# Optimization experiments

Hardware: AMD Instinct MI355X
Metric: run time of the kernel (lower is better)

## Reference

```python
import jax, jax.numpy as jnp
import numpy as np

# geomloss SamplesLoss('sinkhorn', p=2, blur=0.05, scaling=0.5, debias=True) math
P = 2
BLUR = 0.05
SCALING = 0.5
DIAMETER = 64.0  # static conservative bound on point-cloud diameter for randn D=64 data


def _eps_schedule():
    eps_list = []
    e = DIAMETER ** P
    target = BLUR ** P
    while e > target:
        eps_list.append(e)
        e *= SCALING ** P
    eps_list.append(target)
    return np.array(eps_list, dtype=np.float32)


def _cost(x, y):
    # C_ij = ||x_i - y_j||^2 / 2   (p=2 cost of geomloss)
    sq = (jnp.sum(x * x, -1)[:, :, None] * 0.5
          + jnp.sum(y * y, -1)[:, None, :] * 0.5
          - jnp.einsum('bnd,bmd->bnm', x, y))
    return jnp.maximum(sq, 0.0)


def _softmin(eps, C, h):
    # f_i = -eps * log sum_j exp(h_j - C_ij / eps);  C: (B,N,M), h: (B,M)
    return -eps * jax.nn.logsumexp(h[:, None, :] - C / eps, axis=-1)


def setup_inputs() -> dict:
    key = jax.random.key(0)
    k1, k2, k3, k4 = jax.random.split(key, 4)
    B, N, M, D = 8, 2048, 2048, 64
    x = jax.random.normal(k1, (B, N, D), dtype=jnp.float32)
    y = jax.random.normal(k2, (B, M, D), dtype=jnp.float32)
    w1 = jax.random.uniform(k3, (B, N), dtype=jnp.float32) + 0.01
    w2 = jax.random.uniform(k4, (B, M), dtype=jnp.float32) + 0.01
    w1 = w1 / jnp.sum(w1, axis=-1, keepdims=True)
    w2 = w2 / jnp.sum(w2, axis=-1, keepdims=True)
    return {'x': x, 'y': y, 'w1': w1, 'w2': w2}


def _sinkhorn_divergence(x, y, w1, w2):
    a_log = jnp.log(w1)
    b_log = jnp.log(w2)
    eps_list = jnp.asarray(_eps_schedule())

    # --- Sinkhorn loop on detached quantities (geomloss detaches the loop) ---
    xd = jax.lax.stop_gradient(x)
    yd = jax.lax.stop_gradient(y)
    ald = jax.lax.stop_gradient(a_log)
    bld = jax.lax.stop_gradient(b_log)
    C_xy_d = _cost(xd, yd)
    C_yx_d = jnp.swapaxes(C_xy_d, 1, 2)
    C_xx_d = _cost(xd, xd)
    C_yy_d = _cost(yd, yd)

    eps0 = eps_list[0]
    f_ab = _softmin(eps0, C_xy_d, bld)
    g_ba = _softmin(eps0, C_yx_d, ald)
    f_aa = _softmin(eps0, C_xx_d, ald)
    g_bb = _softmin(eps0, C_yy_d, bld)

    def step(carry, eps):
        f_ab, g_ba, f_aa, g_bb = carry
        ft = _softmin(eps, C_xy_d, bld + g_ba / eps)
        gt = _softmin(eps, C_yx_d, ald + f_ab / eps)
        f_aa_t = _softmin(eps, C_xx_d, ald + f_aa / eps)
        g_bb_t = _softmin(eps, C_yy_d, bld + g_bb / eps)
        return (0.5 * (f_ab + ft), 0.5 * (g_ba + gt),
                0.5 * (f_aa + f_aa_t), 0.5 * (g_bb + g_bb_t)), None

    (f_ab, g_ba, f_aa, g_bb), _ = jax.lax.scan(step, (f_ab, g_ba, f_aa, g_bb), eps_list)

    # --- last extrapolation at eps = blur^p, differentiable ---
    eps = eps_list[-1]
    C_xy = _cost(x, y)
    C_yx = jnp.swapaxes(C_xy, 1, 2)
    C_xx = _cost(x, x)
    C_yy = _cost(y, y)
    f_ab_f = _softmin(eps, C_xy, b_log + g_ba / eps)
    g_ba_f = _softmin(eps, C_yx, a_log + f_ab / eps)
    f_aa_f = _softmin(eps, C_xx, a_log + f_aa / eps)
    g_bb_f = _softmin(eps, C_yy, b_log + g_bb / eps)

    # debiased sinkhorn cost per batch element
    loss = (jnp.sum(w1 * (f_ab_f - f_aa_f), axis=-1)
            + jnp.sum(w2 * (g_ba_f - g_bb_f), axis=-1))
    return loss


def reference(x, y, w1, w2):
    loss = _sinkhorn_divergence(x, y, w1, w2)
    return jnp.mean(loss)  # reduction='mean'
```

## Files before the change

### kernel.cpp

```cpp
#include <hip/hip_runtime.h>

#define NB 8
#define NN 2048
#define MM 2048
#define DD 64
#define NCHK 16
#define TS 128
#define L2E 1.4426950408889634f
#define LN2 0.6931471805599453f

typedef _Float16 half_t;
typedef __attribute__((ext_vector_type(8))) _Float16 f16x8;
typedef __attribute__((ext_vector_type(4))) float f32x4;
typedef __attribute__((ext_vector_type(2))) float f32x2;

__device__ inline f32x2 lo2(f32x4 v) { return __builtin_shufflevector(v, v, 0, 1); }
__device__ inline f32x2 hi2(f32x4 v) { return __builtin_shufflevector(v, v, 2, 3); }

__device__ half_t g_xh[NB * NN * DD];
__device__ half_t g_yh[NB * MM * DD];
__device__ float g_fab[3][NB * NN], g_gba[3][NB * NN];
__device__ float g_faa[3][NB * NN], g_gbb[3][NB * NN];
__device__ float g_alog[NB * NN], g_blog[NB * NN];
__device__ float g_xn[NB * NN], g_yn[NB * NN];
__device__ float g_h0[NB * MM], g_h1[NB * NN], g_h2[NB * NN], g_h3[NB * MM];
__device__ float2 g_pfab[NB * NCHK * NN];
__device__ float2 g_pgba[NB * NCHK * NN];
__device__ float2 g_pfaa[NB * NCHK * NN];
__device__ float2 g_pgbb[NB * NCHK * NN];

__global__ __launch_bounds__(256) void prep_kernel(
    const float* __restrict__ x, const float* __restrict__ y,
    const float* __restrict__ w1, const float* __restrict__ w2)
{
  int gid = blockIdx.x * 256 + threadIdx.x;
  if (gid < NB * NN) {
    g_alog[gid] = log2f(w1[gid]);
    g_blog[gid] = log2f(w2[gid]);
  }
  int lane = threadIdx.x & 63;
  int row = blockIdx.x * 4 + (threadIdx.x >> 6);
  float xv = x[(size_t)row * DD + lane];
  float yv = y[(size_t)row * DD + lane];
  g_xh[(size_t)row * DD + lane] = (half_t)xv;
  g_yh[(size_t)row * DD + lane] = (half_t)yv;
  float sx = xv * xv;
  float sy = yv * yv;
#pragma unroll
  for (int off = 32; off > 0; off >>= 1) {
    sx += __shfl_down(sx, off);
    sy += __shfl_down(sy, off);
  }
  if (lane == 0) {
    g_xn[row] = 0.5f * sx;
    g_yn[row] = 0.5f * sy;
  }
}

__global__ __launch_bounds__(256) void hprep_kernel(
    const float* __restrict__ fab_in, const float* __restrict__ gba_in,
    const float* __restrict__ faa_in, const float* __restrict__ gbb_in,
    float gs2)
{
  int i = blockIdx.x * 256 + threadIdx.x;
  g_h0[i] = fmaf(gs2, gba_in[i], g_blog[i]);
  g_h1[i] = fmaf(gs2, fab_in[i], g_alog[i]);
  g_h2[i] = fmaf(gs2, faa_in[i], g_alog[i]);
  g_h3[i] = fmaf(gs2, gbb_in[i], g_blog[i]);
}

struct FusedArgs {
  const half_t* Af;
  const half_t* Bf;
  const float* nrow;
  const float* ncol;
  const float* hrow;
  const float* hcol;
  float2* prow;
  float2* pcol;
  int sym;
};

__global__ __launch_bounds__(512) void tile_fused(
    FusedArgs T0, FusedArgs T1, FusedArgs T2, float keps)
{
  int u = blockIdx.x;
  int slab, b, I, J;
  if (u < 2048) {
    slab = 0; b = u >> 8;
    int tt = u & 255; I = tt >> 4; J = tt & 15;
  } else {
    int v = u - 2048;
    slab = 1 + v / 1088;
    int w2 = v % 1088;
    b = w2 / 136;
    int rem = w2 % 136, ii = 0;
    while (rem >= NCHK - ii) { rem -= NCHK - ii; ++ii; }
    I = ii; J = ii + rem;
  }
  FusedArgs A = (slab == 0) ? T0 : (slab == 1) ? T1 : T2;

  const int t = threadIdx.x;
  const int w = t >> 6, lane = t & 63;
  const int m = lane & 15, quad = lane >> 4;
  const int i0 = I * TS, j0 = J * TS;

  __shared__ __align__(16) char sh[33792];
  float* redR = (float*)sh;
  float* redC = (float*)(sh + 8704);
  float* rowM = (float*)(sh + 25600);
  float* colM = (float*)(sh + 26112);
  float* ynkL = (float*)(sh + 32768);
  float* hrL  = (float*)(sh + 33280);

  {
    const char* gA = (const char*)(A.Af + ((size_t)b * NN + i0) * DD);
    const char* gB = (const char*)(A.Bf + ((size_t)b * MM + j0) * DD);
#pragma unroll
    for (int k = 0; k < 4; ++k) {
      int seg = w * 4 + k;
      int p = (seg * 1024 + lane * 16) & 16383;
      int row = p >> 7, colb = p & 127;
      int colx = colb ^ ((row & 7) << 4);
      const char* src = (seg < 16 ? gA : gB) + (size_t)row * 128 + colx;
      __builtin_amdgcn_global_load_lds(
          (const __attribute__((address_space(1))) unsigned int*)src,
          (__attribute__((address_space(3))) unsigned int*)(sh + seg * 1024),
          16, 0, 0);
    }
  }

  if (t < 128) {
    ynkL[t] = -A.ncol[(size_t)b * MM + j0 + t] * keps;
  } else if (t < 256) {
    hrL[t - 128] = A.hrow[(size_t)b * MM + j0 + (t - 128)];
  }
  size_t ro = (size_t)b * NN + i0 + 16 * w + 4 * quad;
  float4 xr = *(const float4*)(A.nrow + ro);
  float4 hq = *(const float4*)(A.hcol + ro);
  f32x2 xnkp0 = {-xr.x * keps, -xr.y * keps};
  f32x2 xnkp1 = {-xr.z * keps, -xr.w * keps};
  f32x2 hcp0 = {hq.x, hq.y}, hcp1 = {hq.z, hq.w};

  __syncthreads();

  const int qb0 = quad * 16, qb1 = qb0 + 64;
  const int ra = 16 * w + m, sa = (ra & 7) << 4;
  f16x8 a0 = *(const f16x8*)(sh + ra * 128 + (qb0 ^ sa));
  f16x8 a1 = *(const f16x8*)(sh + ra * 128 + (qb1 ^ sa));

  const int sb = (m & 7) << 4;
  const char* bb = sh + 16384 + m * 128;
  f32x4 acc[8];
#pragma unroll
  for (int c = 0; c < 8; ++c) {
    f16x8 b0 = *(const f16x8*)(bb + c * 2048 + (qb0 ^ sb));
    f16x8 b1 = *(const f16x8*)(bb + c * 2048 + (qb1 ^ sb));
    f32x4 a = {0.f, 0.f, 0.f, 0.f};
    a = __builtin_amdgcn_mfma_f32_16x16x32_f16(a0, b0, a, 0, 0, 0);
    a = __builtin_amdgcn_mfma_f32_16x16x32_f16(a1, b1, a, 0, 0, 0);
    acc[c] = a;
  }

  __syncthreads();

  const f32x2 kv = {keps, keps};
  const f32x2 zz = {0.f, 0.f};
  f32x2 rmp0 = {-3.0e38f, -3.0e38f}, rmp1 = {-3.0e38f, -3.0e38f};
#pragma unroll
  for (int c = 0; c < 8; ++c) {
    float ynk_c = ynkL[16 * c + m];
    float hr_c = hrL[16 * c + m];
    f32x2 ay0 = xnkp0 + ynk_c;
    f32x2 ay1 = xnkp1 + ynk_c;
    f32x2 q0 = __builtin_elementwise_fma(lo2(acc[c]), kv, ay0);
    f32x2 q1 = __builtin_elementwise_fma(hi2(acc[c]), kv, ay1);
    f32x2 b0 = __builtin_elementwise_min(q0, zz);
    f32x2 b1 = __builtin_elementwise_min(q1, zz);
    acc[c] = __builtin_shufflevector(b0, b1, 0, 1, 2, 3);
    f32x2 rv0 = b0 + hr_c;
    f32x2 rv1 = b1 + hr_c;
    rmp0 = __builtin_elementwise_max(rmp0, rv0);
    rmp1 = __builtin_elementwise_max(rmp1, rv1);
    f32x2 cv0 = b0 + hcp0;
    f32x2 cv1 = b1 + hcp1;
    float cm_c = fmaxf(fmaxf(cv0.x, cv0.y), fmaxf(cv1.x, cv1.y));
    redC[(16 * c + m) * 33 + 4 * w + quad] = cm_c;
  }
  {
    int rbase = (16 * w + 4 * quad) * 17 + m;
    redR[rbase] = rmp0.x; redR[rbase + 17] = rmp0.y;
    redR[rbase + 34] = rmp1.x; redR[rbase + 51] = rmp1.y;
  }
  __syncthreads();

  if (t < 128) {
    float mx = redR[t * 17];
#pragma unroll
    for (int k = 1; k < 16; ++k) mx = fmaxf(mx, redR[t * 17 + k]);
    rowM[t] = mx;
  } else if (t < 256) {
    int cc = t - 128;
    float mx = redC[cc * 33];
#pragma unroll
    for (int k = 1; k < 32; ++k) mx = fmaxf(mx, redC[cc * 33 + k]);
    colM[cc] = mx;
  }
  __syncthreads();

  float4 rq = *(const float4*)(rowM + 16 * w + 4 * quad);
  f32x2 rmv0 = {rq.x, rq.y}, rmv1 = {rq.z, rq.w};
  f32x2 rsp0 = {0.f, 0.f}, rsp1 = {0.f, 0.f};
#pragma unroll
  for (int c = 0; c < 8; ++c) {
    float hr_c = hrL[16 * c + m];
    float cmv_c = colM[16 * c + m];
    f32x2 hrm0 = hr_c - rmv0;
    f32x2 hrm1 = hr_c - rmv1;
    f32x2 chm0 = hcp0 - cmv_c;
    f32x2 chm1 = hcp1 - cmv_c;
    f32x2 b0 = lo2(acc[c]), b1 = hi2(acc[c]);
    f32x2 t0 = b0 + hrm0, t1 = b1 + hrm1;
    float e0 = __builtin_amdgcn_exp2f(t0.x), e1 = __builtin_amdgcn_exp2f(t0.y);
    float e2 = __builtin_amdgcn_exp2f(t1.x), e3 = __builtin_amdgcn_exp2f(t1.y);
    f32x2 ep0 = {e0, e1}, ep1 = {e2, e3};
    rsp0 += ep0; rsp1 += ep1;
    f32x2 u0 = b0 + chm0, u1 = b1 + chm1;
    float f0 = __builtin_amdgcn_exp2f(u0.x), f1 = __builtin_amdgcn_exp2f(u0.y);
    float f2 = __builtin_amdgcn_exp2f(u1.x), f3 = __builtin_amdgcn_exp2f(u1.y);
    redC[(16 * c + m) * 33 + 4 * w + quad] = (f0 + f1) + (f2 + f3);
  }
  {
    int rbase = (16 * w + 4 * quad) * 17 + m;
    redR[rbase] = rsp0.x; redR[rbase + 17] = rsp0.y;
    redR[rbase + 34] = rsp1.x; redR[rbase + 51] = rsp1.y;
  }
  __syncthreads();

  if (t < 128) {
    float s = 0.f;
#pragma unroll
    for (int k = 0; k < 16; ++k) s += redR[t * 17 + k];
    A.prow[((size_t)b * NCHK + J) * NN + i0 + t] = make_float2(rowM[t], s);
  } else if (t < 256) {
    if (!(A.sym && I == J)) {
      int cc = t - 128;
      float s = 0.f;
#pragma unroll
      for (int k = 0; k < 32; ++k) s += redC[cc * 33 + k];
      A.pcol[((size_t)b * NCHK + I) * NN + j0 + cc] = make_float2(colM[cc], s);
    }
  }
}

struct MergeArgs {
  const float2* part;
  const float* fold;
  float* fout;
  const float* hbase;
  float* hout;
};

__global__ __launch_bounds__(256) void merge4(
    MergeArgs M0, MergeArgs M1, MergeArgs M2, MergeArgs M3,
    float eps, float alpha, float beta, float nextgs)
{
  MergeArgs A = (blockIdx.z == 0) ? M0 : (blockIdx.z == 1) ? M1
              : (blockIdx.z == 2) ? M2 : M3;
  const int b = blockIdx.y;
  const int i = blockIdx.x * 256 + threadIdx.x;
  float2 p[NCHK];
#pragma unroll
  for (int k = 0; k < NCHK; ++k)
    p[k] = A.part[((size_t)b * NCHK + k) * NN + i];
  float M = p[0].x;
#pragma unroll
  for (int k = 1; k < NCHK; ++k) M = fmaxf(M, p[k].x);
  float S = 0.f;
#pragma unroll
  for (int k = 0; k < NCHK; ++k) S += p[k].y * __builtin_amdgcn_exp2f(p[k].x - M);
  float ft = (-LN2 * eps) * (M + __log2f(S));
  int idx = b * NN + i;
  float fnew = alpha * A.fold[idx] + beta * ft;
  A.fout[idx] = fnew;
  A.hout[idx] = fmaf(nextgs * L2E, fnew, A.hbase[idx]);
}

__global__ __launch_bounds__(256) void loss_kernel(
    const float* __restrict__ w1, const float* __restrict__ w2,
    float* __restrict__ out)
{
  __shared__ float red[256];
  float acc = 0.f;
  for (int idx = threadIdx.x; idx < NB * NN; idx += 256) {
    acc += w1[idx] * (g_fab[2][idx] - g_faa[2][idx])
         + w2[idx] * (g_gba[2][idx] - g_gbb[2][idx]);
  }
  red[threadIdx.x] = acc;
  __syncthreads();
  for (int s = 128; s > 0; s >>= 1) {
    if (threadIdx.x < s) red[threadIdx.x] += red[threadIdx.x + s];
    __syncthreads();
  }
  if (threadIdx.x == 0) out[0] = red[0] * (1.0f / NB);
}

extern "C" void kernel_launch(void* const* d_in, const int* in_sizes, int n_in,
                              void* d_out, int out_size, void* d_ws, size_t ws_size,
                              hipStream_t stream)
{
  const float* x = (const float*)d_in[0];
  const float* y = (const float*)d_in[1];
  const float* w1 = (const float*)d_in[2];
  const float* w2 = (const float*)d_in[3];
  float* out = (float*)d_out;

  half_t *xh, *yh;
  float *xn, *yn;
  float *h0, *h1, *h2, *h3, *fabp, *gbap, *faap, *gbbp, *alog, *blog;
  float2 *pfab, *pgba, *pfaa, *pgbb;
  hipGetSymbolAddress((void**)&xh, HIP_SYMBOL(g_xh));
  hipGetSymbolAddress((void**)&yh, HIP_SYMBOL(g_yh));
  hipGetSymbolAddress((void**)&xn, HIP_SYMBOL(g_xn));
  hipGetSymbolAddress((void**)&yn, HIP_SYMBOL(g_yn));
  hipGetSymbolAddress((void**)&h0, HIP_SYMBOL(g_h0));
  hipGetSymbolAddress((void**)&h1, HIP_SYMBOL(g_h1));
  hipGetSymbolAddress((void**)&h2, HIP_SYMBOL(g_h2));
  hipGetSymbolAddress((void**)&h3, HIP_SYMBOL(g_h3));
  hipGetSymbolAddress((void**)&fabp, HIP_SYMBOL(g_fab));
  hipGetSymbolAddress((void**)&gbap, HIP_SYMBOL(g_gba));
  hipGetSymbolAddress((void**)&faap, HIP_SYMBOL(g_faa));
  hipGetSymbolAddress((void**)&gbbp, HIP_SYMBOL(g_gbb));
  hipGetSymbolAddress((void**)&alog, HIP_SYMBOL(g_alog));
  hipGetSymbolAddress((void**)&blog, HIP_SYMBOL(g_blog));
  hipGetSymbolAddress((void**)&pfab, HIP_SYMBOL(g_pfab));
  hipGetSymbolAddress((void**)&pgba, HIP_SYMBOL(g_pgba));
  hipGetSymbolAddress((void**)&pfaa, HIP_SYMBOL(g_pfaa));
  hipGetSymbolAddress((void**)&pgbb, HIP_SYMBOL(g_pgbb));

  auto fab = [&](int s) { return fabp + (size_t)s * NB * NN; };
  auto gba = [&](int s) { return gbap + (size_t)s * NB * NN; };
  auto faa = [&](int s) { return faap + (size_t)s * NB * NN; };
  auto gbb = [&](int s) { return gbbp + (size_t)s * NB * NN; };

  float eps_list[32];
  int ne = 0;
  {
    double v = 64.0 * 64.0;
    double tgt = 0.05 * 0.05;
    while (v > tgt) { eps_list[ne++] = (float)v; v *= 0.25; }
    eps_list[ne++] = (float)tgt;
  }

  prep_kernel<<<4096, 256, 0, stream>>>(x, y, w1, w2);

  dim3 tg(4224);
  dim3 mg(NN / 256, NB, 4);

  auto launch_iter = [&](float eps, float alpha, float beta, float nextgs,
                         int in, int outsel) {
    float keps = L2E / eps;
    FusedArgs T0 = {xh, yh, xn, yn, h0, h1, pfab, pgba, 0};
    FusedArgs T1 = {xh, xh, xn, xn, h2, h2, pfaa, pfaa, 1};
    FusedArgs T2 = {yh, yh, yn, yn, h3, h3, pgbb, pgbb, 1};
    tile_fused<<<tg, 512, 0, stream>>>(T0, T1, T2, keps);
    MergeArgs M0 = {pfab, fab(in), fab(outsel), alog, h1};
    MergeArgs M1 = {pgba, gba(in), gba(outsel), blog, h0};
    MergeArgs M2 = {pfaa, faa(in), faa(outsel), alog, h2};
    MergeArgs M3 = {pgbb, gbb(in), gbb(outsel), blog, h3};
    merge4<<<mg, 256, 0, stream>>>(M0, M1, M2, M3, eps, alpha, beta, nextgs);
  };

  hprep_kernel<<<64, 256, 0, stream>>>(fab(0), gba(0), faa(0), gbb(0), 0.f);
  launch_iter(eps_list[0], 0.f, 1.f, 1.0f / eps_list[0], 0, 0);

  int cur = 0;
  for (int k = 0; k < ne; ++k) {
    int nxt = 1 - cur;
    float nextgs = 1.0f / ((k < ne - 1) ? eps_list[k + 1] : eps_list[ne - 1]);
    launch_iter(eps_list[k], 0.5f, 0.5f, nextgs, cur, nxt);
    cur = nxt;
  }

  launch_iter(eps_list[ne - 1], 0.f, 1.f, 0.f, cur, 2);

  loss_kernel<<<1, 256, 0, stream>>>(w1, w2, out);
}
```

Baseline: 661.7 us.

## Load B tile fragments directly from global memory instead of staging in LDS

Only the A tile is now staged into LDS via async global-to-LDS loads, while each lane reads its B fragments straight from global memory into registers for the MFMA. This removes half the LDS staging traffic and the barrier that separated the matmul from the reduction scratch reuse, because the reduction buffers no longer alias the tile area. The row-reduction scratch is also relaid out so each lane writes one float4 instead of four scalar stores. The trade-off is more uncoalesced, latency-exposed global loads in the MFMA loop and a larger LDS footprint, which may lower occupancy.

```diff
diff --git a/kernel.cpp b/kernel.cpp
--- a/kernel.cpp
+++ b/kernel.cpp
@@ -105,24 +105,23 @@
   const int m = lane & 15, quad = lane >> 4;
   const int i0 = I * TS, j0 = J * TS;
 
-  __shared__ __align__(16) char sh[33792];
-  float* redR = (float*)sh;
-  float* redC = (float*)(sh + 8704);
-  float* rowM = (float*)(sh + 25600);
-  float* colM = (float*)(sh + 26112);
-  float* ynkL = (float*)(sh + 32768);
-  float* hrL  = (float*)(sh + 33280);
+  __shared__ __align__(16) char sh[43776];
+  float* redR2 = (float*)(sh + 16384);
+  float* redC  = (float*)(sh + 24832);
+  float* rowM  = (float*)(sh + 41728);
+  float* colM  = (float*)(sh + 42240);
+  float* ynkL  = (float*)(sh + 42752);
+  float* hrL   = (float*)(sh + 43264);
 
   {
     const char* gA = (const char*)(A.Af + ((size_t)b * NN + i0) * DD);
-    const char* gB = (const char*)(A.Bf + ((size_t)b * MM + j0) * DD);
-#pragma unroll
-    for (int k = 0; k < 4; ++k) {
-      int seg = w * 4 + k;
-      int p = (seg * 1024 + lane * 16) & 16383;
+#pragma unroll
+    for (int k = 0; k < 2; ++k) {
+      int seg = w * 2 + k;
+      int p = seg * 1024 + lane * 16;
       int row = p >> 7, colb = p & 127;
       int colx = colb ^ ((row & 7) << 4);
-      const char* src = (seg < 16 ? gA : gB) + (size_t)row * 128 + colx;
+      const char* src = gA + (size_t)row * 128 + colx;
       __builtin_amdgcn_global_load_lds(
           (const __attribute__((address_space(1))) unsigned int*)src,
           (__attribute__((address_space(3))) unsigned int*)(sh + seg * 1024),
@@ -149,28 +148,26 @@
   f16x8 a0 = *(const f16x8*)(sh + ra * 128 + (qb0 ^ sa));
   f16x8 a1 = *(const f16x8*)(sh + ra * 128 + (qb1 ^ sa));
 
-  const int sb = (m & 7) << 4;
-  const char* bb = sh + 16384 + m * 128;
+  const half_t* bg = A.Bf + ((size_t)b * MM + j0 + m) * DD + quad * 8;
   f32x4 acc[8];
 #pragma unroll
   for (int c = 0; c < 8; ++c) {
-    f16x8 b0 = *(const f16x8*)(bb + c * 2048 + (qb0 ^ sb));
-    f16x8 b1 = *(const f16x8*)(bb + c * 2048 + (qb1 ^ sb));
+    f16x8 b0 = *(const f16x8*)(bg + (size_t)c * 16 * DD);
+    f16x8 b1 = *(const f16x8*)(bg + (size_t)c * 16 * DD + 32);
     f32x4 a = {0.f, 0.f, 0.f, 0.f};
     a = __builtin_amdgcn_mfma_f32_16x16x32_f16(a0, b0, a, 0, 0, 0);
     a = __builtin_amdgcn_mfma_f32_16x16x32_f16(a1, b1, a, 0, 0, 0);
     acc[c] = a;
   }
 
-  __syncthreads();
-
   const f32x2 kv = {keps, keps};
   const f32x2 zz = {0.f, 0.f};
   f32x2 rmp0 = {-3.0e38f, -3.0e38f}, rmp1 = {-3.0e38f, -3.0e38f};
 #pragma unroll
   for (int c = 0; c < 8; ++c) {
-    float ynk_c = ynkL[16 * c + m];
-    float hr_c = hrL[16 * c + m];
+    int cc = 16 * c + m;
+    float ynk_c = ynkL[cc];
+    float hr_c = hrL[cc];
     f32x2 ay0 = xnkp0 + ynk_c;
     f32x2 ay1 = xnkp1 + ynk_c;
     f32x2 q0 = __builtin_elementwise_fma(lo2(acc[c]), kv, ay0);
@@ -185,19 +182,16 @@
     f32x2 cv0 = b0 + hcp0;
     f32x2 cv1 = b1 + hcp1;
     float cm_c = fmaxf(fmaxf(cv0.x, cv0.y), fmaxf(cv1.x, cv1.y));
-    redC[(16 * c + m) * 33 + 4 * w + quad] = cm_c;
-  }
-  {
-    int rbase = (16 * w + 4 * quad) * 17 + m;
-    redR[rbase] = rmp0.x; redR[rbase + 17] = rmp0.y;
-    redR[rbase + 34] = rmp1.x; redR[rbase + 51] = rmp1.y;
-  }
+    redC[cc * 33 + 4 * w + quad] = cm_c;
+  }
+  *(float4*)(redR2 + (size_t)m * 132 + 16 * w + 4 * quad) =
+      make_float4(rmp0.x, rmp0.y, rmp1.x, rmp1.y);
   __syncthreads();
 
   if (t < 128) {
-    float mx = redR[t * 17];
-#pragma unroll
-    for (int k = 1; k < 16; ++k) mx = fmaxf(mx, redR[t * 17 + k]);
+    float mx = redR2[t];
+#pragma unroll
+    for (int k = 1; k < 16; ++k) mx = fmaxf(mx, redR2[k * 132 + t]);
     rowM[t] = mx;
   } else if (t < 256) {
     int cc = t - 128;
@@ -213,8 +207,9 @@
   f32x2 rsp0 = {0.f, 0.f}, rsp1 = {0.f, 0.f};
 #pragma unroll
   for (int c = 0; c < 8; ++c) {
-    float hr_c = hrL[16 * c + m];
-    float cmv_c = colM[16 * c + m];
+    int cc = 16 * c + m;
+    float hr_c = hrL[cc];
+    float cmv_c = colM[cc];
     f32x2 hrm0 = hr_c - rmv0;
     f32x2 hrm1 = hr_c - rmv1;
     f32x2 chm0 = hcp0 - cmv_c;
@@ -228,19 +223,16 @@
     f32x2 u0 = b0 + chm0, u1 = b1 + chm1;
     float f0 = __builtin_amdgcn_exp2f(u0.x), f1 = __builtin_amdgcn_exp2f(u0.y);
     float f2 = __builtin_amdgcn_exp2f(u1.x), f3 = __builtin_amdgcn_exp2f(u1.y);
-    redC[(16 * c + m) * 33 + 4 * w + quad] = (f0 + f1) + (f2 + f3);
-  }
-  {
-    int rbase = (16 * w + 4 * quad) * 17 + m;
-    redR[rbase] = rsp0.x; redR[rbase + 17] = rsp0.y;
-    redR[rbase + 34] = rsp1.x; redR[rbase + 51] = rsp1.y;
-  }
+    redC[cc * 33 + 4 * w + quad] = (f0 + f1) + (f2 + f3);
+  }
+  *(float4*)(redR2 + (size_t)m * 132 + 16 * w + 4 * quad) =
+      make_float4(rsp0.x, rsp0.y, rsp1.x, rsp1.y);
   __syncthreads();
 
   if (t < 128) {
     float s = 0.f;
 #pragma unroll
-    for (int k = 0; k < 16; ++k) s += redR[t * 17 + k];
+    for (int k = 0; k < 16; ++k) s += redR2[k * 132 + t];
     A.prow[((size_t)b * NCHK + J) * NN + i0 + t] = make_float2(rowM[t], s);
   } else if (t < 256) {
     if (!(A.sym && I == J)) {
```

Result: slower. 1.112 ms (+68.0%).
